# Performance work log

Measured on AMD Instinct MI355X. Metric: run time of the kernel, lower is better.

## Reference

```python
import jax, jax.numpy as jnp
import numpy as np

B, N, M, C, H, G, KD = 4, 1024, 128, 512, 8, 3, 16
DH = C // H


def setup_inputs() -> dict:
    key = jax.random.key(0)
    ks = jax.random.split(key, 12)
    def w(k, shape, fan_in):
        return jax.random.normal(k, shape, jnp.float32) / np.sqrt(fan_in)
    return {
        'pairwise_g': jax.random.normal(ks[0], (B, N, N, G), jnp.float32),
        'coset_functions': jax.random.normal(ks[1], (B, N, C), jnp.float32),
        'mask': jnp.ones((B, N), dtype=bool),
        'W1': w(ks[2], (G, KD), G), 'b1': jnp.zeros((KD,), jnp.float32),
        'W2': w(ks[3], (KD, KD), KD), 'b2': jnp.zeros((KD,), jnp.float32),
        'W3': w(ks[4], (KD, H), KD), 'b3': jnp.zeros((H,), jnp.float32),
        'Wq': w(ks[5], (C, C), C), 'bq': jnp.zeros((C,), jnp.float32),
        'Wk': w(ks[6], (C, C), C), 'bk': jnp.zeros((C,), jnp.float32),
        'Wv': w(ks[7], (C, C), C), 'bv': jnp.zeros((C,), jnp.float32),
        'Wo': w(ks[8], (C, C), C), 'bo': jnp.zeros((C,), jnp.float32),
    }


def _gather_nbhd(x, idx):
    # x: (B, N, ...) gathered along point axis with idx: (B, Nq, M) -> (B, Nq, M, ...)
    return jax.vmap(lambda a, i: a[i])(x, idx)


def reference(pairwise_g, coset_functions, mask,
              W1, b1, W2, b2, W3, b3,
              Wq, bq, Wk, bk, Wv, bv, Wo, bo):
    swish = jax.nn.silu
    # --- neighborhood extraction: topk smallest group distance (mc_samples path) ---
    dists = jnp.linalg.norm(pairwise_g, axis=-1)                  # (B,N,N)
    dists = jnp.where(mask[:, None, :], dists, jnp.float32(1e8))
    _, nbhd_idx = jax.lax.top_k(-dists, M)                        # (B,N,M) nearest M

    nbhd_g = jnp.take_along_axis(pairwise_g, nbhd_idx[..., None], axis=2)  # (B,N,M,G)
    nbhd_mask = _gather_nbhd(mask, nbhd_idx)                      # (B,N,M)

    # --- location kernel: per-pair MLP on lie-algebra offsets -> per-head logits ---
    h = swish(nbhd_g @ W1 + b1)
    h = swish(h @ W2 + b2)
    loc = h @ W3 + b3                                             # (B,N,M,H)

    # --- feature kernel: multi-head dot product, keys gathered at neighborhoods ---
    q = (coset_functions @ Wq + bq).reshape(B, N, H, DH)
    k = coset_functions @ Wk + bk                                 # (B,N,C)
    k_n = _gather_nbhd(k, nbhd_idx).reshape(B, N, M, H, DH)
    dot = jnp.einsum('bnhd,bnmhd->bnmh', q, k_n) / jnp.sqrt(jnp.float32(DH))

    # --- masked softmax over neighborhood axis ---
    pre = loc + dot
    pre = jnp.where(nbhd_mask[..., None], pre, jnp.float32(-1e38))
    attn = jax.nn.softmax(pre, axis=2)                            # (B,N,M,H)

    # --- value projection, gather, weighted aggregate, output projection ---
    v = coset_functions @ Wv + bv                                 # (B,N,C)
    v_n = _gather_nbhd(v, nbhd_idx).reshape(B, N, M, H, DH)
    out = jnp.einsum('bnmh,bnmhd->bnhd', attn, v_n).reshape(B, N, C)
    out = out @ Wo + bo                                           # (B,N,C)
    return out
```

## Files before the change

### kernel.cpp

```cpp
#include <hip/hip_runtime.h>
#include <hip/hip_bf16.h>
#include <math.h>

#define NB 4
#define NPTS 1024
#define MN 128
#define CH 512
#define NH 8
#define DHD 64
#define NG 3
#define KDIM 16

typedef unsigned short u16;
typedef unsigned short u16x8 __attribute__((ext_vector_type(8)));
typedef short short8 __attribute__((ext_vector_type(8)));
typedef float f32x4 __attribute__((ext_vector_type(4)));
typedef float f32x2 __attribute__((ext_vector_type(2)));

#define FEXP(x) __expf(x)

#if defined(__has_builtin)
#if __has_builtin(__builtin_amdgcn_fdot2_f32_bf16)
#define HAS_DOT2 1
typedef __bf16 bf16x2 __attribute__((ext_vector_type(2)));
#endif
#endif

__device__ __forceinline__ float b2f(u16 u) {
  return __uint_as_float(((unsigned)u) << 16);
}
__device__ __forceinline__ u16 f2b(float f) {
  unsigned x = __float_as_uint(f);
  return (u16)((x + 0x7FFFu + ((x >> 16) & 1u)) >> 16);
}
__device__ __forceinline__ f32x2 bpair(unsigned u) {
  f32x2 r;
  r.x = __uint_as_float(u << 16);
  r.y = __uint_as_float(u & 0xFFFF0000u);
  return r;
}

__global__ __launch_bounds__(256) void cvt_bf16(const float* __restrict__ x,
                                                u16* __restrict__ y) {
  int i = blockIdx.x * 256 + threadIdx.x;
  float4 a = ((const float4*)x)[i * 2];
  float4 b = ((const float4*)x)[i * 2 + 1];
  ushort4 o0, o1;
  o0.x = f2b(a.x); o0.y = f2b(a.y); o0.z = f2b(a.z); o0.w = f2b(a.w);
  o1.x = f2b(b.x); o1.y = f2b(b.y); o1.z = f2b(b.z); o1.w = f2b(b.w);
  ((ushort4*)y)[i * 2] = o0;
  ((ushort4*)y)[i * 2 + 1] = o1;
}

__global__ __launch_bounds__(256) void transpose_cvt(
    const float* __restrict__ W0, const float* __restrict__ W1,
    const float* __restrict__ W2, const float* __restrict__ W3,
    u16* __restrict__ T0, u16* __restrict__ T1, u16* __restrict__ T2,
    u16* __restrict__ T3) {
  const float* src; u16* dst;
  if (blockIdx.z == 0)      { src = W0; dst = T0; }
  else if (blockIdx.z == 1) { src = W1; dst = T1; }
  else if (blockIdx.z == 2) { src = W2; dst = T2; }
  else                      { src = W3; dst = T3; }
  __shared__ float tile[32][33];
  const int k0 = blockIdx.y * 32, n0 = blockIdx.x * 32;
  const int r8 = threadIdx.x >> 5, c = threadIdx.x & 31;
#pragma unroll
  for (int i = 0; i < 4; i++)
    tile[r8 + i * 8][c] = src[(size_t)(k0 + r8 + i * 8) * CH + n0 + c];
  __syncthreads();
#pragma unroll
  for (int i = 0; i < 4; i++)
    dst[(size_t)(n0 + r8 + i * 8) * CH + k0 + c] = f2b(tile[c][r8 + i * 8]);
}

__device__ __forceinline__ void gstore(float* p, float v) { *p = v; }
__device__ __forceinline__ void gstore(u16* p, float v) { *p = f2b(v); }

template <typename OT>
__global__ __launch_bounds__(256) void mfma_gemm3(
    const u16* __restrict__ A,
    const u16* __restrict__ Wa, const float* __restrict__ ba,
    const u16* __restrict__ Wb, const float* __restrict__ bb_,
    const u16* __restrict__ Wc, const float* __restrict__ bc,
    OT* __restrict__ Ya, OT* __restrict__ Yb, OT* __restrict__ Yc) {
  const u16* W; const float* bias; OT* Y;
  if (blockIdx.z == 0)      { W = Wa; bias = ba;  Y = Ya; }
  else if (blockIdx.z == 1) { W = Wb; bias = bb_; Y = Yb; }
  else                      { W = Wc; bias = bc;  Y = Yc; }

  __shared__ u16 As[128][40];
  __shared__ u16 Bs[128][40];

  const int t = threadIdx.x;
  const int row0 = blockIdx.y * 128;
  const int col0 = blockIdx.x * 128;
  const int r2 = t >> 1;
  const int sb = (t & 1) * 16;
  const int w = t >> 6, lane = t & 63;
  const int q4 = lane >> 4, l16 = lane & 15;
  const int wr = (w & 1) * 64, wc = (w >> 1) * 64;

  f32x4 acc[4][4];
#pragma unroll
  for (int mt = 0; mt < 4; mt++)
#pragma unroll
    for (int nt = 0; nt < 4; nt++) acc[mt][nt] = (f32x4){0.f, 0.f, 0.f, 0.f};

  for (int kt = 0; kt < CH; kt += 32) {
    u16x8 av0 = *(const u16x8*)(A + (size_t)(row0 + r2) * CH + kt + sb);
    u16x8 av1 = *(const u16x8*)(A + (size_t)(row0 + r2) * CH + kt + sb + 8);
    u16x8 bv0 = *(const u16x8*)(W + (size_t)(col0 + r2) * CH + kt + sb);
    u16x8 bv1 = *(const u16x8*)(W + (size_t)(col0 + r2) * CH + kt + sb + 8);
    *(u16x8*)&As[r2][sb] = av0;
    *(u16x8*)&As[r2][sb + 8] = av1;
    *(u16x8*)&Bs[r2][sb] = bv0;
    *(u16x8*)&Bs[r2][sb + 8] = bv1;
    __syncthreads();
    short8 af[4], bf[4];
#pragma unroll
    for (int mt = 0; mt < 4; mt++)
      af[mt] = *(const short8*)&As[wr + mt * 16 + l16][q4 * 8];
#pragma unroll
    for (int nt = 0; nt < 4; nt++)
      bf[nt] = *(const short8*)&Bs[wc + nt * 16 + l16][q4 * 8];
#pragma unroll
    for (int mt = 0; mt < 4; mt++)
#pragma unroll
      for (int nt = 0; nt < 4; nt++)
        acc[mt][nt] = __builtin_amdgcn_mfma_f32_16x16x32_bf16(
            af[mt], bf[nt], acc[mt][nt], 0, 0, 0);
    __syncthreads();
  }

#pragma unroll
  for (int nt = 0; nt < 4; nt++) {
    const int col = col0 + wc + nt * 16 + l16;
    const float bb = bias[col];
#pragma unroll
    for (int mt = 0; mt < 4; mt++) {
#pragma unroll
      for (int r = 0; r < 4; r++) {
        const int row = row0 + wr + mt * 16 + q4 * 4 + r;
        gstore(Y + (size_t)row * CH + col, acc[mt][nt][r] + bb);
      }
    }
  }
}

__global__ __launch_bounds__(256) void select_loc(
    const float* __restrict__ g, int* __restrict__ idx_out,
    const float* __restrict__ W1, const float* __restrict__ b1,
    const float* __restrict__ W2, const float* __restrict__ b2,
    const float* __restrict__ W3, const float* __restrict__ b3,
    u16* __restrict__ locw) {
  const int bn = blockIdx.x;
  const int t = threadIdx.x;
  const int wv = t >> 6, lane = t & 63;
  __shared__ unsigned int key[NPTS];
  __shared__ int hist[4][256];
  __shared__ int incl[256];
  __shared__ int wtot[4];
  __shared__ int selidx[MN];
  __shared__ unsigned int s_prefix;
  __shared__ unsigned int s_selmask;
  __shared__ int s_target, s_done, s_cless, s_ctie, s_fill;

  const float* row = g + (size_t)bn * (NPTS * NG);
#pragma unroll
  for (int r = 0; r < 4; r++) {
    int j = t + 256 * r;
    float g0 = row[j * 3 + 0];
    float g1 = row[j * 3 + 1];
    float g2 = row[j * 3 + 2];
    float ss = __fadd_rn(__fadd_rn(__fmul_rn(g0, g0), __fmul_rn(g1, g1)),
                         __fmul_rn(g2, g2));
    key[j] = __float_as_uint(__fsqrt_rn(ss));
  }
  if (t == 0) {
    s_prefix = 0u; s_target = MN - 1; s_done = 0;
    s_selmask = 0xFFFFFFFFu;
  }
  __syncthreads();

  for (int pass = 3; pass >= 0; pass--) {
    if (s_done) break;
    const unsigned int pref = s_prefix;
    const int target = s_target;
    const int sh = 8 * pass;
    const unsigned int himask = (pass == 3) ? 0u : (0xFFFFFFFFu << (sh + 8));
#pragma unroll
    for (int w = 0; w < 4; w++) hist[w][t] = 0;
    __syncthreads();
#pragma unroll
    for (int r = 0; r < 4; r++) {
      unsigned int kk = key[t + 256 * r];
      if ((kk & himask) == (pref & himask))
        atomicAdd(&hist[wv][(kk >> sh) & 255], 1);
    }
    __syncthreads();
    int sv = hist[0][t] + hist[1][t] + hist[2][t] + hist[3][t];
#pragma unroll
    for (int o = 1; o < 64; o <<= 1) {
      int n = __shfl_up(sv, o);
      if (lane >= o) sv += n;
    }
    if (lane == 63) wtot[wv] = sv;
    __syncthreads();
    int base = 0;
#pragma unroll
    for (int w = 0; w < 4; w++) base += (w < wv) ? wtot[w] : 0;
    sv += base;
    incl[t] = sv;
    __syncthreads();
    int below = (t == 0) ? 0 : incl[t - 1];
    int mine = incl[t];
    __syncthreads();
    if (mine > target && below <= target) {
      s_prefix = pref | ((unsigned int)t << sh);
      s_target = target - below;
      if (mine - below == target - below + 1) {
        s_done = 1;
        s_selmask = 0xFFFFFFFFu << sh;
      }
    }
    __syncthreads();
  }

  const unsigned int sm = s_selmask;
  const unsigned int T = s_prefix;
  const int need = s_target + 1;
  if (t == 0) { s_cless = 0; s_ctie = 0; s_fill = 0; }
  __syncthreads();
  int* orow = idx_out + bn * MN;
#pragma unroll
  for (int r = 0; r < 4; r++) {
    int j = t + 256 * r;
    unsigned int kk = key[j] & sm;
    if (kk < T) {
      int p = atomicAdd(&s_cless, 1);
      if (p < MN) { orow[p] = j; selidx[p] = j; }
    } else if (kk == T) {
      atomicAdd(&s_ctie, 1);
    }
  }
  __syncthreads();
  const int L = s_cless;
  const int ctie = s_ctie;
  __syncthreads();
  if (ctie == need) {
    for (int r = 0; r < 4; r++) {
      int j = t + 256 * r;
      if ((key[j] & sm) == T) {
        int p = atomicAdd(&s_fill, 1);
        int q = L + p;
        if (q < MN) { orow[q] = j; selidx[q] = j; }
      }
    }
  } else {
    for (int r = 0; r < 4; r++) {
      int j = t + 256 * r;
      if ((key[j] & sm) == T) {
        int rank = 0;
        for (int jj = 0; jj < j; jj++) rank += ((key[jj] & sm) == T) ? 1 : 0;
        int q = L + rank;
        if (rank < need && q >= 0 && q < MN) { orow[q] = j; selidx[q] = j; }
      }
    }
  }
  __syncthreads();

  if (t < MN) {
    const int j = selidx[t] & (NPTS - 1);
    const float* gp = g + ((size_t)bn * NPTS + j) * NG;
    float g0 = gp[0], g1 = gp[1], g2 = gp[2];
    float h1[KDIM], h2[KDIM];
#pragma unroll
    for (int u = 0; u < KDIM; u++) {
      float s = W1[u] * g0 + W1[KDIM + u] * g1 + W1[2 * KDIM + u] * g2 + b1[u];
      h1[u] = s / (1.f + FEXP(-s));
    }
#pragma unroll
    for (int vv = 0; vv < KDIM; vv++) {
      float s = b2[vv];
#pragma unroll
      for (int u = 0; u < KDIM; u++) s += h1[u] * W2[u * KDIM + vv];
      h2[vv] = s / (1.f + FEXP(-s));
    }
    u16* op = locw + ((size_t)bn * MN + t) * NH;
#pragma unroll
    for (int h = 0; h < NH; h++) {
      float s = b3[h];
#pragma unroll
      for (int vv = 0; vv < KDIM; vv++) s += h2[vv] * W3[vv * NH + h];
      op[h] = f2b(s);
    }
  }
}

__global__ __launch_bounds__(256, 8) void attn_kernel(
    const u16* __restrict__ qg, const u16* __restrict__ kg,
    const u16* __restrict__ vg, const u16* __restrict__ locw,
    const int* __restrict__ idxg, u16* __restrict__ outg) {
  const int t = threadIdx.x;
  const int wv = t >> 6;
  const int lane = t & 63;
  const int pt = wv >> 1;
  const int half = wv & 1;
  const int bn = blockIdx.x * 2 + pt;
  const int b = bn >> 10;

  __shared__ int nidx[2][MN];
  __shared__ float red[2][64][11];

  nidx[pt][half * 64 + lane] = idxg[bn * MN + half * 64 + lane] & (NPTS - 1);
  __syncthreads();

  u16x8 qv = *(const u16x8*)(qg + (size_t)bn * CH + lane * 8);
  const int hl = lane >> 3;
  const u16* kb = kg + (size_t)b * NPTS * CH;
  const u16* vb = vg + (size_t)b * NPTS * CH;
  const u16* lb = locw + (size_t)bn * MN * NH + hl;

  float M = -INFINITY, L = 0.f;
  f32x2 acc[4];
#pragma unroll
  for (int i = 0; i < 4; i++) acc[i] = (f32x2){0.f, 0.f};

#if defined(HAS_DOT2)
  bf16x2 qh[4];
  {
    union { u16x8 v; unsigned u[4]; } uq; uq.v = qv;
#pragma unroll
    for (int i = 0; i < 4; i++) qh[i] = __builtin_bit_cast(bf16x2, uq.u[i]);
  }
#else
  float qf[8];
#pragma unroll
  for (int e = 0; e < 8; e++) qf[e] = b2f(qv[e]);
#endif

  const int mb = half * 64;
  const int* nrow = &nidx[pt][mb];
  for (int mi = 0; mi < 64; mi += 2) {
    const int j0 = nrow[mi];
    const int j1 = nrow[mi + 1];
    u16x8 k0v = *(const u16x8*)(kb + (size_t)j0 * CH + lane * 8);
    u16x8 k1v = *(const u16x8*)(kb + (size_t)j1 * CH + lane * 8);
    u16x8 v0v = *(const u16x8*)(vb + (size_t)j0 * CH + lane * 8);
    u16x8 v1v = *(const u16x8*)(vb + (size_t)j1 * CH + lane * 8);
    float l0 = b2f(lb[(mb + mi) * NH]);
    float l1 = b2f(lb[(mb + mi + 1) * NH]);

    union { u16x8 v; unsigned u[4]; } uk0, uk1, uv0, uv1;
    uk0.v = k0v; uk1.v = k1v; uv0.v = v0v; uv1.v = v1v;

    float p0 = 0.f, p1 = 0.f;
#if defined(HAS_DOT2)
#pragma unroll
    for (int e = 0; e < 4; e++) {
      p0 = __builtin_amdgcn_fdot2_f32_bf16(
          qh[e], __builtin_bit_cast(bf16x2, uk0.u[e]), p0, false);
      p1 = __builtin_amdgcn_fdot2_f32_bf16(
          qh[e], __builtin_bit_cast(bf16x2, uk1.u[e]), p1, false);
    }
#else
#pragma unroll
    for (int e = 0; e < 4; e++) {
      f32x2 kp0 = bpair(uk0.u[e]);
      f32x2 kp1 = bpair(uk1.u[e]);
      p0 += qf[2 * e] * kp0.x + qf[2 * e + 1] * kp0.y;
      p1 += qf[2 * e] * kp1.x + qf[2 * e + 1] * kp1.y;
    }
#endif
    p0 += __shfl_xor(p0, 1); p0 += __shfl_xor(p0, 2); p0 += __shfl_xor(p0, 4);
    p1 += __shfl_xor(p1, 1); p1 += __shfl_xor(p1, 2); p1 += __shfl_xor(p1, 4);
    p0 = p0 * 0.125f + l0;
    p1 = p1 * 0.125f + l1;

    float mx = fmaxf(M, fmaxf(p0, p1));
    float alpha = FEXP(M - mx);
    float e0 = FEXP(p0 - mx);
    float e1 = FEXP(p1 - mx);
    L = L * alpha + e0 + e1;
    const f32x2 av = (f32x2){alpha, alpha};
    const f32x2 e0v = (f32x2){e0, e0};
    const f32x2 e1v = (f32x2){e1, e1};
#pragma unroll
    for (int i = 0; i < 4; i++)
      acc[i] = acc[i] * av + bpair(uv0.u[i]) * e0v + bpair(uv1.u[i]) * e1v;
    M = mx;
  }

  if (half) {
    float* rp = &red[pt][lane][0];
#pragma unroll
    for (int i = 0; i < 4; i++) {
      rp[2 * i] = acc[i].x;
      rp[2 * i + 1] = acc[i].y;
    }
    rp[8] = M;
    rp[9] = L;
  }
  __syncthreads();
  if (!half) {
    const float* rp = &red[pt][lane][0];
    const float M1 = rp[8], L1 = rp[9];
    const float mx = fmaxf(M, M1);
    const float s0 = FEXP(M - mx);
    const float s1 = FEXP(M1 - mx);
    const float inv = 1.f / (L * s0 + L1 * s1);
    u16x8 o;
#pragma unroll
    for (int i = 0; i < 4; i++) {
      o[2 * i] = f2b((acc[i].x * s0 + rp[2 * i] * s1) * inv);
      o[2 * i + 1] = f2b((acc[i].y * s0 + rp[2 * i + 1] * s1) * inv);
    }
    *(u16x8*)(outg + (size_t)bn * CH + lane * 8) = o;
  }
}

extern "C" void kernel_launch(void* const* d_in, const int* in_sizes, int n_in,
                              void* d_out, int out_size, void* d_ws, size_t ws_size,
                              hipStream_t stream) {
  (void)in_sizes; (void)n_in; (void)out_size; (void)ws_size;
  const float* pg = (const float*)d_in[0];
  const float* cf = (const float*)d_in[1];
  const float* W1 = (const float*)d_in[3];
  const float* b1 = (const float*)d_in[4];
  const float* W2 = (const float*)d_in[5];
  const float* b2 = (const float*)d_in[6];
  const float* W3 = (const float*)d_in[7];
  const float* b3 = (const float*)d_in[8];
  const float* Wq = (const float*)d_in[9];
  const float* bq = (const float*)d_in[10];
  const float* Wk = (const float*)d_in[11];
  const float* bk = (const float*)d_in[12];
  const float* Wv = (const float*)d_in[13];
  const float* bv = (const float*)d_in[14];
  const float* Wo = (const float*)d_in[15];
  const float* bo = (const float*)d_in[16];
  float* out = (float*)d_out;

  char* p = (char*)d_ws;
  u16* cfb = (u16*)p;
  u16* WTq = (u16*)(p + (4 << 20));
  u16* WTk = WTq + 262144;
  u16* WTv = WTk + 262144;
  u16* WTo = WTv + 262144;
  u16* qw = (u16*)(p + (6 << 20));
  u16* kw = (u16*)(p + (10 << 20));
  u16* vw = (u16*)(p + (14 << 20));
  int* idxw = (int*)(p + (18 << 20));
  u16* locw = (u16*)(p + (20 << 20));
  u16* awb = qw;

  const int R = NB * NPTS;

  cvt_bf16<<<dim3(R * CH / 8 / 256), 256, 0, stream>>>(cf, cfb);
  transpose_cvt<<<dim3(16, 16, 4), 256, 0, stream>>>(Wq, Wk, Wv, Wo, WTq, WTk,
                                                     WTv, WTo);
  mfma_gemm3<u16><<<dim3(CH / 128, R / 128, 3), 256, 0, stream>>>(
      cfb, WTq, bq, WTk, bk, WTv, bv, qw, kw, vw);
  select_loc<<<dim3(R), 256, 0, stream>>>(pg, idxw, W1, b1, W2, b2, W3, b3,
                                          locw);
  attn_kernel<<<dim3(R / 2), 256, 0, stream>>>(qw, kw, vw, locw, idxw, awb);
  mfma_gemm3<float><<<dim3(CH / 128, R / 128, 1), 256, 0, stream>>>(
      awb, WTo, bo, WTo, bo, WTo, bo, out, out, out);
}
```

Baseline: 233.3 us.

## Remap attention blocks per XCD, shuffle neighbor indices, prefetch next keys

Block indices are remapped so each of the 8 XCDs handles a contiguous range of query points within one batch, which is meant to improve L2 reuse of gathered K/V rows. Neighbor indices are now held in registers and broadcast with wave shuffles instead of being staged through shared memory, which removes a __syncthreads. The K rows for the next iteration are loaded one step ahead to hide gather latency. This costs extra registers and does one wasted wrap-around prefetch at the end.

After: 232.4 us. About the same (-0.4%).

```diff
diff --git a/kernel.cpp b/kernel.cpp
--- a/kernel.cpp
+++ b/kernel.cpp
@@ -307,14 +307,18 @@
   const int lane = t & 63;
   const int pt = wv >> 1;
   const int half = wv & 1;
-  const int bn = blockIdx.x * 2 + pt;
+
+  const int i = blockIdx.x;
+  const int xcd = i & 7;
+  const int ord = i >> 3;
+  const int bnpair = (xcd >> 1) * (NPTS / 2) + (xcd & 1) * 256 + ord;
+  const int bn = bnpair * 2 + pt;
   const int b = bn >> 10;
 
-  __shared__ int nidx[2][MN];
   __shared__ float red[2][64][11];
 
-  nidx[pt][half * 64 + lane] = idxg[bn * MN + half * 64 + lane] & (NPTS - 1);
-  __syncthreads();
+  const int mb = half * 64;
+  const int myj = idxg[bn * MN + mb + lane] & (NPTS - 1);
 
   u16x8 qv = *(const u16x8*)(qg + (size_t)bn * CH + lane * 8);
   const int hl = lane >> 3;
@@ -325,14 +329,14 @@
   float M = -INFINITY, L = 0.f;
   f32x2 acc[4];
 #pragma unroll
-  for (int i = 0; i < 4; i++) acc[i] = (f32x2){0.f, 0.f};
+  for (int i2 = 0; i2 < 4; i2++) acc[i2] = (f32x2){0.f, 0.f};
 
 #if defined(HAS_DOT2)
   bf16x2 qh[4];
   {
     union { u16x8 v; unsigned u[4]; } uq; uq.v = qv;
 #pragma unroll
-    for (int i = 0; i < 4; i++) qh[i] = __builtin_bit_cast(bf16x2, uq.u[i]);
+    for (int i2 = 0; i2 < 4; i2++) qh[i2] = __builtin_bit_cast(bf16x2, uq.u[i2]);
   }
 #else
   float qf[8];
@@ -340,20 +344,24 @@
   for (int e = 0; e < 8; e++) qf[e] = b2f(qv[e]);
 #endif
 
-  const int mb = half * 64;
-  const int* nrow = &nidx[pt][mb];
+  int j0 = __shfl(myj, 0);
+  int j1 = __shfl(myj, 1);
+  u16x8 k0v = *(const u16x8*)(kb + (size_t)j0 * CH + lane * 8);
+  u16x8 k1v = *(const u16x8*)(kb + (size_t)j1 * CH + lane * 8);
+
   for (int mi = 0; mi < 64; mi += 2) {
-    const int j0 = nrow[mi];
-    const int j1 = nrow[mi + 1];
-    u16x8 k0v = *(const u16x8*)(kb + (size_t)j0 * CH + lane * 8);
-    u16x8 k1v = *(const u16x8*)(kb + (size_t)j1 * CH + lane * 8);
+    const int nm = (mi + 2) & 63;
+    const int j0n = __shfl(myj, nm);
+    const int j1n = __shfl(myj, nm + 1);
+    u16x8 k0n = *(const u16x8*)(kb + (size_t)j0n * CH + lane * 8);
+    u16x8 k1n = *(const u16x8*)(kb + (size_t)j1n * CH + lane * 8);
     u16x8 v0v = *(const u16x8*)(vb + (size_t)j0 * CH + lane * 8);
     u16x8 v1v = *(const u16x8*)(vb + (size_t)j1 * CH + lane * 8);
     float l0 = b2f(lb[(mb + mi) * NH]);
     float l1 = b2f(lb[(mb + mi + 1) * NH]);
 
     union { u16x8 v; unsigned u[4]; } uk0, uk1, uv0, uv1;
-    uk0.v = k0v; uk1.v = k1v; uv0.v = v0v; uv1.v = v1v;
+    uk0.v = k0v; uk1.v = k1v;
 
     float p0 = 0.f, p1 = 0.f;
 #if defined(HAS_DOT2)
@@ -383,21 +391,24 @@
     float e0 = FEXP(p0 - mx);
     float e1 = FEXP(p1 - mx);
     L = L * alpha + e0 + e1;
+    uv0.v = v0v; uv1.v = v1v;
     const f32x2 av = (f32x2){alpha, alpha};
     const f32x2 e0v = (f32x2){e0, e0};
     const f32x2 e1v = (f32x2){e1, e1};
 #pragma unroll
-    for (int i = 0; i < 4; i++)
-      acc[i] = acc[i] * av + bpair(uv0.u[i]) * e0v + bpair(uv1.u[i]) * e1v;
+    for (int i2 = 0; i2 < 4; i2++)
+      acc[i2] = acc[i2] * av + bpair(uv0.u[i2]) * e0v + bpair(uv1.u[i2]) * e1v;
     M = mx;
+
+    k0v = k0n; k1v = k1n; j0 = j0n; j1 = j1n;
   }
 
   if (half) {
     float* rp = &red[pt][lane][0];
 #pragma unroll
-    for (int i = 0; i < 4; i++) {
-      rp[2 * i] = acc[i].x;
-      rp[2 * i + 1] = acc[i].y;
+    for (int i2 = 0; i2 < 4; i2++) {
+      rp[2 * i2] = acc[i2].x;
+      rp[2 * i2 + 1] = acc[i2].y;
     }
     rp[8] = M;
     rp[9] = L;
@@ -412,9 +423,9 @@
     const float inv = 1.f / (L * s0 + L1 * s1);
     u16x8 o;
 #pragma unroll
-    for (int i = 0; i < 4; i++) {
-      o[2 * i] = f2b((acc[i].x * s0 + rp[2 * i] * s1) * inv);
-      o[2 * i + 1] = f2b((acc[i].y * s0 + rp[2 * i + 1] * s1) * inv);
+    for (int i2 = 0; i2 < 4; i2++) {
+      o[2 * i2] = f2b((acc[i2].x * s0 + rp[2 * i2] * s1) * inv);
+      o[2 * i2 + 1] = f2b((acc[i2].y * s0 + rp[2 * i2 + 1] * s1) * inv);
     }
     *(u16x8*)(outg + (size_t)bn * CH + lane * 8) = o;
   }
```
